# Optimization experiments

Hardware: AMD Instinct MI355X
Metric: run time of the kernel (lower is better)

## Reference

```python
import jax, jax.numpy as jnp
import numpy as np
from jax import lax

B, L = 16, 2048
D_TOK, D_TIS = 256, 64
D_MODEL = D_TOK + D_TIS          # 320
EXPAND = 2
D_INNER = EXPAND * D_MODEL       # 640
D_STATE = 16
D_CONV = 4
DT_RANK = (D_MODEL + 15) // 16   # 20 (ceil(d_model/16), Mamba default)
H_OUT = 128
VOCAB = 65                       # len(CODON_MAP_DNA)+1
N_TISSUES = 30
MAX_NORM = 2.0


def _embed_maxnorm(W, idx):
    # torch nn.Embedding(max_norm=2): looked-up rows are renormalized to norm<=2
    e = W[idx]
    n = jnp.linalg.norm(e, axis=-1, keepdims=True)
    return e * jnp.minimum(1.0, MAX_NORM / jnp.maximum(n, 1e-12))


def setup_inputs() -> dict:
    key = jax.random.key(0)
    ks = jax.random.split(key, 18)
    s = 0.02
    seq_W = jax.random.normal(ks[3], (VOCAB, D_TOK), dtype=jnp.float32)
    seq_W = seq_W.at[0].set(0.0)  # padding_idx=0
    A_log = jnp.log(jnp.broadcast_to(jnp.arange(1, D_STATE + 1, dtype=jnp.float32), (D_INNER, D_STATE)))
    return {
        "rna_data_pad": jax.random.randint(ks[0], (B, L), 0, VOCAB).astype(jnp.int32),
        "tissue_id": jax.random.randint(ks[1], (B,), 0, N_TISSUES).astype(jnp.int32),
        "seq_lengths": jax.random.randint(ks[2], (B,), 1, L + 1).astype(jnp.int32),
        "seq_W": seq_W,
        "tissue_W": jax.random.normal(ks[4], (N_TISSUES, D_TIS), dtype=jnp.float32),
        "in_proj_W": jax.random.normal(ks[5], (2 * D_INNER, D_MODEL), dtype=jnp.float32) * s,
        "conv_w": jax.random.normal(ks[6], (D_INNER, 1, D_CONV), dtype=jnp.float32) * s,
        "conv_b": jnp.zeros((D_INNER,), dtype=jnp.float32),
        "x_proj_W": jax.random.normal(ks[7], (DT_RANK + 2 * D_STATE, D_INNER), dtype=jnp.float32) * s,
        "dt_proj_W": jax.random.normal(ks[8], (D_INNER, DT_RANK), dtype=jnp.float32) * s,
        "dt_proj_b": jax.random.uniform(ks[9], (D_INNER,), minval=-4.0, maxval=-2.0),
        "A_log": A_log,
        "D_skip": jnp.ones((D_INNER,), dtype=jnp.float32),
        "out_proj_W": jax.random.normal(ks[10], (D_MODEL, D_INNER), dtype=jnp.float32) * s,
        "p1_W": jax.random.normal(ks[11], (H_OUT, D_MODEL), dtype=jnp.float32) * s,
        "p1_b": jnp.zeros((H_OUT,), dtype=jnp.float32),
        "p2_W": jax.random.normal(ks[12], (1, H_OUT), dtype=jnp.float32) * s,
        "p2_b": jnp.zeros((1,), dtype=jnp.float32),
    }


def reference(rna_data_pad, tissue_id, seq_lengths, seq_W, tissue_W, in_proj_W,
              conv_w, conv_b, x_proj_W, dt_proj_W, dt_proj_b, A_log, D_skip,
              out_proj_W, p1_W, p1_b, p2_W, p2_b):
    b, l = rna_data_pad.shape
    # embeddings + tissue broadcast + mask
    seq_emb = _embed_maxnorm(seq_W, rna_data_pad)            # [B,L,D_TOK]
    tis_emb = _embed_maxnorm(tissue_W, tissue_id)            # [B,D_TIS]
    tis_exp = jnp.broadcast_to(tis_emb[:, None, :], (b, l, tis_emb.shape[-1]))
    x = jnp.concatenate([seq_emb, tis_exp], axis=-1)          # [B,L,D_MODEL]
    x = x * (rna_data_pad != 0)[..., None]
    # Mamba block
    xz = x @ in_proj_W.T                                      # [B,L,2*D_INNER]
    xm, z = jnp.split(xz, 2, axis=-1)
    xt = xm.transpose(0, 2, 1)                                # [B,D_INNER,L]
    conv = lax.conv_general_dilated(
        xt, conv_w, window_strides=(1,), padding=[(D_CONV - 1, 0)],
        feature_group_count=D_INNER,
        dimension_numbers=("NCH", "OIH", "NCH")) + conv_b[None, :, None]
    xm = jax.nn.silu(conv).transpose(0, 2, 1)                 # [B,L,D_INNER]
    x_dbl = xm @ x_proj_W.T                                   # [B,L,DT_RANK+2*D_STATE]
    dt, Bm, Cm = jnp.split(x_dbl, [DT_RANK, DT_RANK + D_STATE], axis=-1)
    delta = jax.nn.softplus(dt @ dt_proj_W.T + dt_proj_b)     # [B,L,D_INNER]
    A = -jnp.exp(A_log)                                       # [D_INNER,D_STATE]
    # selective scan over time
    xs = (delta.transpose(1, 0, 2), Bm.transpose(1, 0, 2),
          Cm.transpose(1, 0, 2), xm.transpose(1, 0, 2))
    h0 = jnp.zeros((b, D_INNER, D_STATE), dtype=xm.dtype)

    def step(h, t):
        dl, bt, ct, ut = t                                    # [B,di],[B,ds],[B,ds],[B,di]
        dA = jnp.exp(dl[:, :, None] * A)                      # [B,di,ds]
        dBu = (dl * ut)[:, :, None] * bt[:, None, :]          # [B,di,ds]
        h = dA * h + dBu
        y = jnp.einsum("bds,bs->bd", h, ct)
        return h, y

    _, ys = lax.scan(step, h0, xs)                            # ys: [L,B,D_INNER]
    y = ys.transpose(1, 0, 2) + xm * D_skip
    y = y * jax.nn.silu(z)
    out = y @ out_proj_W.T                                    # [B,L,D_MODEL]
    # gather last valid timestep
    out_last = out[jnp.arange(b), seq_lengths - 1]            # [B,D_MODEL]
    h1 = jax.nn.relu(out_last @ p1_W.T + p1_b)
    return h1 @ p2_W.T + p2_b                                 # [B,1]
```

## Files before the change

### kernel.cpp

```cpp
#include <hip/hip_runtime.h>
#include <hip/hip_bf16.h>
#include <math.h>

#define B_      16
#define L_      2048
#define D_MODEL 320
#define D_INNER 640
#define D_STATE 16
#define DT_RANK 20
#define H_OUT   128
#define VOCAB   65
#define N_TIS   30
#define TT      8
#define ST      64
#define NCHUNK  16
#define CHLEN   (L_/NCHUNK)

static constexpr size_t OFF_MSEQ  = 0;
static constexpr size_t OFF_MTIS  = OFF_MSEQ + VOCAB*1280;
static constexpr size_t OFF_YSCAN = OFF_MTIS + N_TIS*1280;
static constexpr size_t OFF_CLAST = OFF_YSCAN + B_*D_INNER;
static constexpr size_t OFF_XD    = OFF_CLAST + B_*16;
static constexpr size_t OFF_PC    = OFF_XD + (size_t)B_*L_*36;
static constexpr size_t OFF_SC    = OFF_PC + (size_t)B_*NCHUNK*40*256;

__device__ __forceinline__ float silu_f(float x) { return x / (1.0f + __expf(-x)); }

__global__ __launch_bounds__(256) void k_mbuild(
    const float* __restrict__ seqW, const float* __restrict__ tisW,
    const float* __restrict__ inW, float* __restrict__ ws)
{
    __shared__ float a_l[256];
    __shared__ float red[4];
    int v = blockIdx.x, tid = threadIdx.x;
    int K, wofs; const float* src; float* dstM;
    if (v < VOCAB) { K = 256; wofs = 0;   src = seqW + (size_t)v*256;        dstM = ws + OFF_MSEQ + (size_t)v*1280; }
    else           { K = 64;  wofs = 256; src = tisW + (size_t)(v-VOCAB)*64; dstM = ws + OFF_MTIS + (size_t)(v-VOCAB)*1280; }
    float x = (tid < K) ? src[tid] : 0.0f;
    float ss = x * x;
    #pragma unroll
    for (int o = 32; o; o >>= 1) ss += __shfl_xor(ss, o);
    if ((tid & 63) == 0) red[tid >> 6] = ss;
    __syncthreads();
    float tot = red[0] + red[1] + red[2] + red[3];
    float scale = fminf(1.0f, 2.0f / fmaxf(sqrtf(tot), 1e-12f));
    if (tid < K) a_l[tid] = x * scale;
    __syncthreads();

    int j = blockIdx.y * 256 + tid;
    const float* w = inW + (size_t)j*320 + wofs;
    float ac0 = 0.f, ac1 = 0.f, ac2 = 0.f, ac3 = 0.f;
    #pragma unroll 4
    for (int k = 0; k < K; k += 4) {
        float4 w4 = *(const float4*)(w + k);
        ac0 += a_l[k+0]*w4.x; ac1 += a_l[k+1]*w4.y;
        ac2 += a_l[k+2]*w4.z; ac3 += a_l[k+3]*w4.w;
    }
    dstM[j] = (ac0 + ac1) + (ac2 + ac3);
}

__global__ __launch_bounds__(256) void k_xdbl(
    const int* __restrict__ idx, const int* __restrict__ tissue_id,
    const int* __restrict__ seq_lengths,
    const float* __restrict__ conv_w, const float* __restrict__ conv_b,
    const float* __restrict__ xW, float* __restrict__ ws)
{
    __shared__ float u_l[TT*641];
    __shared__ float xd_l[TT*36];
    __shared__ int   idx_l[TT+3];
    int b = blockIdx.y;
    int t0 = blockIdx.x * TT;
    int t_last = seq_lengths[b] - 1;
    if (t0 > t_last) return;
    int tid = threadIdx.x;
    const float* Mseq = ws + OFF_MSEQ;
    const float* Mtis = ws + OFF_MTIS;
    int tis = tissue_id[b];
    if (tid < TT+3) {
        int t = t0 - 3 + tid;
        idx_l[tid] = (t >= 0) ? idx[b*L_ + t] : 0;
    }
    __syncthreads();

    for (int d = tid; d < D_INNER; d += 256) {
        float w0 = conv_w[d*4+0], w1 = conv_w[d*4+1], w2 = conv_w[d*4+2], w3 = conv_w[d*4+3];
        float cb = conv_b[d];
        float mt = Mtis[(size_t)tis*1280 + d];
        auto XZ = [&](int k) -> float {
            int row = idx_l[k];
            return row ? (Mseq[(size_t)row*1280 + d] + mt) : 0.0f;
        };
        float a0 = XZ(0), a1 = XZ(1), a2 = XZ(2);
        for (int t = 0; t < TT; ++t) {
            float a3 = XZ(t+3);
            float c = w0*a0 + w1*a1 + w2*a2 + w3*a3 + cb;
            u_l[t*641 + d] = silu_f(c);
            a0 = a1; a1 = a2; a2 = a3;
        }
    }
    __syncthreads();

    {
        int w = tid >> 6, l = tid & 63;
        #pragma unroll 1
        for (int pass = 0; pass < 3; ++pass) {
            float wreg[3][10];
            #pragma unroll
            for (int kk = 0; kk < 3; ++kk) {
                const float* xr = xW + (size_t)(w + 4*(3*pass + kk))*D_INNER + l;
                #pragma unroll
                for (int i = 0; i < 10; ++i) wreg[kk][i] = xr[64*i];
            }
            for (int t = 0; t < TT; ++t) {
                float ur[10];
                #pragma unroll
                for (int i = 0; i < 10; ++i) ur[i] = u_l[t*641 + l + 64*i];
                #pragma unroll
                for (int kk = 0; kk < 3; ++kk) {
                    float p = 0.f;
                    #pragma unroll
                    for (int i = 0; i < 10; ++i) p = fmaf(wreg[kk][i], ur[i], p);
                    #pragma unroll
                    for (int o = 32; o; o >>= 1) p += __shfl_xor(p, o);
                    if (l == t) xd_l[t*36 + w + 4*(3*pass + kk)] = p;
                }
            }
        }
        if (t_last < t0 + TT) {
            int tl = t_last - t0;
            float ur[10];
            #pragma unroll
            for (int i = 0; i < 10; ++i) ur[i] = u_l[tl*641 + l + 64*i];
            #pragma unroll
            for (int k = 0; k < 4; ++k) {
                const float* xr = xW + (size_t)(36 + w + 4*k)*D_INNER + l;
                float p = 0.f;
                #pragma unroll
                for (int i = 0; i < 10; ++i) p = fmaf(xr[64*i], ur[i], p);
                #pragma unroll
                for (int o = 32; o; o >>= 1) p += __shfl_xor(p, o);
                if (l == 0) ws[OFF_CLAST + b*16 + w + 4*k] = p;
            }
        }
    }
    __syncthreads();

    {
        int tmax = min(TT-1, t_last - t0);
        int cnt = (tmax + 1) * 36;
        float* dst = ws + OFF_XD + ((size_t)b*L_ + t0)*36;
        for (int o = tid; o < cnt; o += 256) dst[o] = xd_l[o];
    }
}

__global__ __launch_bounds__(256) void k_scanc(
    const int* __restrict__ idx, const int* __restrict__ tissue_id,
    const int* __restrict__ seq_lengths,
    const float* __restrict__ conv_w, const float* __restrict__ conv_b,
    const float* __restrict__ dtW, const float* __restrict__ dtb,
    const float* __restrict__ A_log, float* __restrict__ ws)
{
    __shared__ float xd_t[ST*36];
    __shared__ float dl_t[16*68];
    __shared__ float du_t[16*68];
    __shared__ float dtw_l[16*20];
    __shared__ float cw_l[16*4];
    __shared__ float cb_l[16], dtb_l[16], mt_l[16];
    __shared__ int   idx_t[ST+3];

    int b = blockIdx.y, dg = blockIdx.x, c = blockIdx.z;
    int t_last = seq_lengths[b] - 1;
    int t_begin = c * CHLEN;
    if (t_begin > t_last) return;
    int t_end = min(t_begin + CHLEN - 1, t_last);
    int tid = threadIdx.x;
    int dl = tid >> 4, s = tid & 15;
    int tis = tissue_id[b];
    const float* Mseq = ws + OFF_MSEQ;

    if (tid < 16) {
        int d = dg*16 + tid;
        cb_l[tid]  = conv_b[d];
        dtb_l[tid] = dtb[d];
        mt_l[tid]  = ws[OFF_MTIS + (size_t)tis*1280 + d];
    }
    if (tid < 64) {
        int dd = tid >> 2, k = tid & 3;
        cw_l[dd*4 + k] = conv_w[(dg*16 + dd)*4 + k];
    }
    for (int o = tid; o < 16*20; o += 256) {
        int dd = o / 20, r = o % 20;
        dtw_l[o] = dtW[(dg*16 + dd)*20 + r];
    }
    float A = -__expf(A_log[(dg*16 + dl)*D_STATE + s]);

    float h = 0.0f;
    float sd = 0.0f;
    for (int t0 = t_begin; t0 <= t_end; t0 += ST) {
        int nt = min(ST, t_end - t0 + 1);
        if (tid < ST+3) {
            int t = t0 - 3 + tid;
            idx_t[tid] = (t >= 0 && t < L_) ? idx[b*L_ + t] : 0;
        }
        {
            const float* src = ws + OFF_XD + ((size_t)b*L_ + t0)*36;
            int cnt = nt * 36;
            for (int o = tid; o < cnt; o += 256) xd_t[o] = src[o];
        }
        __syncthreads();

        {
            int tt = tid >> 2, dd0 = (tid & 3) * 4;
            if (tt < nt) {
                float cc0 = cb_l[dd0+0], cc1 = cb_l[dd0+1], cc2 = cb_l[dd0+2], cc3 = cb_l[dd0+3];
                #pragma unroll
                for (int k = 0; k < 4; ++k) {
                    int row = idx_t[tt + k];
                    float4 m;
                    if (row) {
                        m = *(const float4*)(Mseq + (size_t)row*1280 + dg*16 + dd0);
                        m.x += mt_l[dd0+0]; m.y += mt_l[dd0+1];
                        m.z += mt_l[dd0+2]; m.w += mt_l[dd0+3];
                    } else m = make_float4(0.f,0.f,0.f,0.f);
                    cc0 = fmaf(cw_l[(dd0+0)*4+k], m.x, cc0);
                    cc1 = fmaf(cw_l[(dd0+1)*4+k], m.y, cc1);
                    cc2 = fmaf(cw_l[(dd0+2)*4+k], m.z, cc2);
                    cc3 = fmaf(cw_l[(dd0+3)*4+k], m.w, cc3);
                }
                float uu[4] = { silu_f(cc0), silu_f(cc1), silu_f(cc2), silu_f(cc3) };
                float xdr[20];
                #pragma unroll
                for (int r = 0; r < 20; ++r) xdr[r] = xd_t[tt*36 + r];
                #pragma unroll
                for (int i = 0; i < 4; ++i) {
                    int d = dd0 + i;
                    float x = dtb_l[d];
                    #pragma unroll
                    for (int r = 0; r < 20; ++r) x = fmaf(xdr[r], dtw_l[d*20 + r], x);
                    float sp = fmaxf(x, 0.0f) + log1pf(__expf(-fabsf(x)));
                    dl_t[d*68 + tt] = sp;
                    du_t[d*68 + tt] = sp * uu[i];
                }
            }
        }
        __syncthreads();

        {
            int q4 = nt >> 2;
            for (int q = 0; q < q4; ++q) {
                float4 d4 = *(const float4*)(dl_t + dl*68 + 4*q);
                float4 u4 = *(const float4*)(du_t + dl*68 + 4*q);
                float b0 = xd_t[(4*q+0)*36 + 20 + s];
                float b1 = xd_t[(4*q+1)*36 + 20 + s];
                float b2 = xd_t[(4*q+2)*36 + 20 + s];
                float b3 = xd_t[(4*q+3)*36 + 20 + s];
                h = fmaf(__expf(d4.x*A), h, u4.x*b0);
                h = fmaf(__expf(d4.y*A), h, u4.y*b1);
                h = fmaf(__expf(d4.z*A), h, u4.z*b2);
                h = fmaf(__expf(d4.w*A), h, u4.w*b3);
                sd += (d4.x + d4.y) + (d4.z + d4.w);
            }
            for (int tt = q4*4; tt < nt; ++tt) {
                float dlt = dl_t[dl*68 + tt];
                h = fmaf(__expf(dlt * A), h, du_t[dl*68 + tt] * xd_t[tt*36 + 20 + s]);
                sd += dlt;
            }
        }
        __syncthreads();
    }
    float P = __expf(A * sd);
    size_t base = (((size_t)b*NCHUNK + c)*40 + dg)*256 + tid;
    ws[OFF_PC + base] = P;
    ws[OFF_SC + base] = h;
}

__global__ __launch_bounds__(256) void k_comb(const int* __restrict__ seq_lengths,
                                              float* __restrict__ ws)
{
    int b = blockIdx.y, dg = blockIdx.x;
    int tid = threadIdx.x;
    int dl = tid >> 4, s = tid & 15;
    int t_last = seq_lengths[b] - 1;
    int ncv = t_last / CHLEN + 1;
    float h = 0.0f;
    for (int c = 0; c < ncv; ++c) {
        size_t base = (((size_t)b*NCHUNK + c)*40 + dg)*256 + tid;
        h = fmaf(ws[OFF_PC + base], h, ws[OFF_SC + base]);
    }
    float v = h * ws[OFF_CLAST + b*16 + s];
    v += __shfl_xor(v, 1); v += __shfl_xor(v, 2);
    v += __shfl_xor(v, 4); v += __shfl_xor(v, 8);
    if (s == 0) ws[OFF_YSCAN + (size_t)b*D_INNER + dg*16 + dl] = v;
}

__global__ __launch_bounds__(320) void k_final(
    const int* __restrict__ idx, const int* __restrict__ tissue_id,
    const int* __restrict__ seq_lengths,
    const float* __restrict__ conv_w, const float* __restrict__ conv_b,
    const float* __restrict__ Dskip, const float* __restrict__ outW,
    const float* __restrict__ p1W, const float* __restrict__ p1b,
    const float* __restrict__ p2W, const float* __restrict__ p2b,
    const float* __restrict__ ws, float* __restrict__ out)
{
    __shared__ float y_l[D_INNER];
    __shared__ float o_l[D_MODEL];
    __shared__ float h1_l[H_OUT];
    int b = blockIdx.x, tid = threadIdx.x;
    int t_last = seq_lengths[b] - 1;
    int tis = tissue_id[b];
    const float* Mseq = ws + OFF_MSEQ;
    const float* Mtis = ws + OFF_MTIS;
    int rows[4];
    #pragma unroll
    for (int k = 0; k < 4; ++k) {
        int t = t_last - 3 + k;
        rows[k] = (t >= 0) ? idx[b*L_ + t] : 0;
    }
    for (int d = tid; d < D_INNER; d += 320) {
        float conv = conv_b[d];
        const float* cw = conv_w + d*4;
        #pragma unroll
        for (int k = 0; k < 4; ++k) {
            int row = rows[k];
            float xz = row ? (Mseq[(size_t)row*1280 + d] + Mtis[(size_t)tis*1280 + d]) : 0.0f;
            conv += cw[k] * xz;
        }
        float u = silu_f(conv);
        int rowL = rows[3];
        float z = rowL ? (Mseq[(size_t)rowL*1280 + 640 + d] + Mtis[(size_t)tis*1280 + 640 + d]) : 0.0f;
        float ys = ws[OFF_YSCAN + (size_t)b*D_INNER + d];
        y_l[d] = (ys + u * Dskip[d]) * silu_f(z);
    }
    __syncthreads();
    if (tid < D_MODEL) {
        const float* w = outW + tid*D_INNER;
        float acc = 0.f;
        #pragma unroll 4
        for (int k = 0; k < D_INNER; k += 4) {
            float4 w4 = *(const float4*)(w + k);
            acc += y_l[k]*w4.x + y_l[k+1]*w4.y + y_l[k+2]*w4.z + y_l[k+3]*w4.w;
        }
        o_l[tid] = acc;
    }
    __syncthreads();
    if (tid < H_OUT) {
        const float* w = p1W + tid*D_MODEL;
        float acc = p1b[tid];
        #pragma unroll 4
        for (int k = 0; k < D_MODEL; k += 4) {
            float4 w4 = *(const float4*)(w + k);
            acc += o_l[k]*w4.x + o_l[k+1]*w4.y + o_l[k+2]*w4.z + o_l[k+3]*w4.w;
        }
        h1_l[tid] = fmaxf(acc, 0.0f);
    }
    __syncthreads();
    if (tid == 0) {
        float acc = p2b[0];
        for (int k = 0; k < H_OUT; ++k) acc += h1_l[k]*p2W[k];
        out[b] = acc;
    }
}

extern "C" void kernel_launch(void* const* d_in, const int* in_sizes, int n_in,
                              void* d_out, int out_size, void* d_ws, size_t ws_size,
                              hipStream_t stream)
{
    const int*   idx   = (const int*)d_in[0];
    const int*   tis   = (const int*)d_in[1];
    const int*   slen  = (const int*)d_in[2];
    const float* seqW  = (const float*)d_in[3];
    const float* tisW  = (const float*)d_in[4];
    const float* inW   = (const float*)d_in[5];
    const float* convw = (const float*)d_in[6];
    const float* convb = (const float*)d_in[7];
    const float* xW    = (const float*)d_in[8];
    const float* dtW   = (const float*)d_in[9];
    const float* dtb   = (const float*)d_in[10];
    const float* Alog  = (const float*)d_in[11];
    const float* Dsk   = (const float*)d_in[12];
    const float* outW  = (const float*)d_in[13];
    const float* p1W   = (const float*)d_in[14];
    const float* p1b   = (const float*)d_in[15];
    const float* p2W   = (const float*)d_in[16];
    const float* p2b   = (const float*)d_in[17];
    float* ws  = (float*)d_ws;
    float* out = (float*)d_out;

    hipLaunchKernelGGL(k_mbuild, dim3(VOCAB + N_TIS, 5), dim3(256), 0, stream, seqW, tisW, inW, ws);
    hipLaunchKernelGGL(k_xdbl,   dim3(L_/TT, B_),        dim3(256), 0, stream,
                       idx, tis, slen, convw, convb, xW, ws);
    hipLaunchKernelGGL(k_scanc,  dim3(D_INNER/16, B_, NCHUNK), dim3(256), 0, stream,
                       idx, tis, slen, convw, convb, dtW, dtb, Alog, ws);
    hipLaunchKernelGGL(k_comb,   dim3(D_INNER/16, B_),   dim3(256), 0, stream, slen, ws);
    hipLaunchKernelGGL(k_final,  dim3(B_),               dim3(320), 0, stream,
                       idx, tis, slen, convw, convb, Dsk, outW, p1W, p1b, p2W, p2b, ws, out);
}
```

Baseline: 298.8 us.

## Restructure scan-chunk prologue, fold chunk combine into final kernel, use exp2

The per-chunk scan kernel now has each thread own one inner channel and compute four consecutive timesteps. Conv weights, dt weights and biases are held in registers instead of shared memory, and convolution inputs are reused across the sliding window. Loads become float4, softplus uses fast log, and the decay exponent switches to exp2 with a prescaled A. The separate chunk-combine kernel is removed and its work is folded into k_final, saving a launch but serializing the combine over only 16 blocks.

```diff
diff --git a/kernel.cpp b/kernel.cpp
--- a/kernel.cpp
+++ b/kernel.cpp
@@ -161,11 +161,8 @@
     const float* __restrict__ A_log, float* __restrict__ ws)
 {
     __shared__ float xd_t[ST*36];
-    __shared__ float dl_t[16*68];
-    __shared__ float du_t[16*68];
-    __shared__ float dtw_l[16*20];
-    __shared__ float cw_l[16*4];
-    __shared__ float cb_l[16], dtb_l[16], mt_l[16];
+    __shared__ float dl_t[16*72];
+    __shared__ float du_t[16*72];
     __shared__ int   idx_t[ST+3];
 
     int b = blockIdx.y, dg = blockIdx.x, c = blockIdx.z;
@@ -175,24 +172,22 @@
     int t_end = min(t_begin + CHLEN - 1, t_last);
     int tid = threadIdx.x;
     int dl = tid >> 4, s = tid & 15;
+    int dd = tid & 15, tg = tid >> 4;
+    int d_own = dg*16 + dd;
     int tis = tissue_id[b];
     const float* Mseq = ws + OFF_MSEQ;
 
-    if (tid < 16) {
-        int d = dg*16 + tid;
-        cb_l[tid]  = conv_b[d];
-        dtb_l[tid] = dtb[d];
-        mt_l[tid]  = ws[OFF_MTIS + (size_t)tis*1280 + d];
-    }
-    if (tid < 64) {
-        int dd = tid >> 2, k = tid & 3;
-        cw_l[dd*4 + k] = conv_w[(dg*16 + dd)*4 + k];
-    }
-    for (int o = tid; o < 16*20; o += 256) {
-        int dd = o / 20, r = o % 20;
-        dtw_l[o] = dtW[(dg*16 + dd)*20 + r];
-    }
-    float A = -__expf(A_log[(dg*16 + dl)*D_STATE + s]);
+    float dtw_r[20];
+    #pragma unroll
+    for (int i = 0; i < 20; i += 4) {
+        float4 w4 = *(const float4*)(dtW + d_own*20 + i);
+        dtw_r[i] = w4.x; dtw_r[i+1] = w4.y; dtw_r[i+2] = w4.z; dtw_r[i+3] = w4.w;
+    }
+    float4 cw4 = *(const float4*)(conv_w + d_own*4);
+    float  cb  = conv_b[d_own];
+    float  dtb_v = dtb[d_own];
+    float  mt  = ws[OFF_MTIS + (size_t)tis*1280 + d_own];
+    float As = -__expf(A_log[(dg*16 + dl)*D_STATE + s]) * 1.44269504089f;
 
     float h = 0.0f;
     float sd = 0.0f;
@@ -203,43 +198,58 @@
             idx_t[tid] = (t >= 0 && t < L_) ? idx[b*L_ + t] : 0;
         }
         {
-            const float* src = ws + OFF_XD + ((size_t)b*L_ + t0)*36;
-            int cnt = nt * 36;
-            for (int o = tid; o < cnt; o += 256) xd_t[o] = src[o];
+            const float4* src = (const float4*)(ws + OFF_XD + ((size_t)b*L_ + t0)*36);
+            float4* dst = (float4*)xd_t;
+            int cnt4 = nt * 9;
+            for (int o = tid; o < cnt4; o += 256) dst[o] = src[o];
         }
         __syncthreads();
 
         {
-            int tt = tid >> 2, dd0 = (tid & 3) * 4;
-            if (tt < nt) {
-                float cc0 = cb_l[dd0+0], cc1 = cb_l[dd0+1], cc2 = cb_l[dd0+2], cc3 = cb_l[dd0+3];
-                #pragma unroll
-                for (int k = 0; k < 4; ++k) {
-                    int row = idx_t[tt + k];
-                    float4 m;
-                    if (row) {
-                        m = *(const float4*)(Mseq + (size_t)row*1280 + dg*16 + dd0);
-                        m.x += mt_l[dd0+0]; m.y += mt_l[dd0+1];
-                        m.z += mt_l[dd0+2]; m.w += mt_l[dd0+3];
-                    } else m = make_float4(0.f,0.f,0.f,0.f);
-                    cc0 = fmaf(cw_l[(dd0+0)*4+k], m.x, cc0);
-                    cc1 = fmaf(cw_l[(dd0+1)*4+k], m.y, cc1);
-                    cc2 = fmaf(cw_l[(dd0+2)*4+k], m.z, cc2);
-                    cc3 = fmaf(cw_l[(dd0+3)*4+k], m.w, cc3);
+            int ttb = tg * 4;
+            if (ttb < nt) {
+                float xz[7];
+                #pragma unroll
+                for (int k = 0; k < 7; ++k) {
+                    int row = idx_t[ttb + k];
+                    xz[k] = row ? (Mseq[(size_t)row*1280 + d_own] + mt) : 0.0f;
                 }
-                float uu[4] = { silu_f(cc0), silu_f(cc1), silu_f(cc2), silu_f(cc3) };
-                float xdr[20];
-                #pragma unroll
-                for (int r = 0; r < 20; ++r) xdr[r] = xd_t[tt*36 + r];
-                #pragma unroll
-                for (int i = 0; i < 4; ++i) {
-                    int d = dd0 + i;
-                    float x = dtb_l[d];
-                    #pragma unroll
-                    for (int r = 0; r < 20; ++r) x = fmaf(xdr[r], dtw_l[d*20 + r], x);
-                    float sp = fmaxf(x, 0.0f) + log1pf(__expf(-fabsf(x)));
-                    dl_t[d*68 + tt] = sp;
-                    du_t[d*68 + tt] = sp * uu[i];
+                float dl4[4], du4[4];
+                bool full = (ttb + 3 < nt);
+                #pragma unroll
+                for (int j = 0; j < 4; ++j) {
+                    int tt = ttb + j;
+                    if (full || tt < nt) {
+                        float cc = cb;
+                        cc = fmaf(cw4.x, xz[j+0], cc);
+                        cc = fmaf(cw4.y, xz[j+1], cc);
+                        cc = fmaf(cw4.z, xz[j+2], cc);
+                        cc = fmaf(cw4.w, xz[j+3], cc);
+                        float u = silu_f(cc);
+                        const float* xr = xd_t + tt*36;
+                        float x = dtb_v;
+                        #pragma unroll
+                        for (int r = 0; r < 20; r += 4) {
+                            float4 x4 = *(const float4*)(xr + r);
+                            x = fmaf(x4.x, dtw_r[r+0], x);
+                            x = fmaf(x4.y, dtw_r[r+1], x);
+                            x = fmaf(x4.z, dtw_r[r+2], x);
+                            x = fmaf(x4.w, dtw_r[r+3], x);
+                        }
+                        float e = __expf(-fabsf(x));
+                        float sp = fmaxf(x, 0.0f) + __logf(1.0f + e);
+                        dl4[j] = sp;
+                        du4[j] = sp * u;
+                    } else { dl4[j] = 0.f; du4[j] = 0.f; }
+                }
+                if (full) {
+                    *(float4*)(dl_t + dd*72 + ttb) = make_float4(dl4[0], dl4[1], dl4[2], dl4[3]);
+                    *(float4*)(du_t + dd*72 + ttb) = make_float4(du4[0], du4[1], du4[2], du4[3]);
+                } else {
+                    for (int j = 0; j < 4 && ttb + j < nt; ++j) {
+                        dl_t[dd*72 + ttb + j] = dl4[j];
+                        du_t[dd*72 + ttb + j] = du4[j];
+                    }
                 }
             }
         }
@@ -248,49 +258,30 @@
         {
             int q4 = nt >> 2;
             for (int q = 0; q < q4; ++q) {
-                float4 d4 = *(const float4*)(dl_t + dl*68 + 4*q);
-                float4 u4 = *(const float4*)(du_t + dl*68 + 4*q);
+                float4 d4 = *(const float4*)(dl_t + dl*72 + 4*q);
+                float4 u4 = *(const float4*)(du_t + dl*72 + 4*q);
                 float b0 = xd_t[(4*q+0)*36 + 20 + s];
                 float b1 = xd_t[(4*q+1)*36 + 20 + s];
                 float b2 = xd_t[(4*q+2)*36 + 20 + s];
                 float b3 = xd_t[(4*q+3)*36 + 20 + s];
-                h = fmaf(__expf(d4.x*A), h, u4.x*b0);
-                h = fmaf(__expf(d4.y*A), h, u4.y*b1);
-                h = fmaf(__expf(d4.z*A), h, u4.z*b2);
-                h = fmaf(__expf(d4.w*A), h, u4.w*b3);
+                h = fmaf(exp2f(d4.x*As), h, u4.x*b0);
+                h = fmaf(exp2f(d4.y*As), h, u4.y*b1);
+                h = fmaf(exp2f(d4.z*As), h, u4.z*b2);
+                h = fmaf(exp2f(d4.w*As), h, u4.w*b3);
                 sd += (d4.x + d4.y) + (d4.z + d4.w);
             }
             for (int tt = q4*4; tt < nt; ++tt) {
-                float dlt = dl_t[dl*68 + tt];
-                h = fmaf(__expf(dlt * A), h, du_t[dl*68 + tt] * xd_t[tt*36 + 20 + s]);
+                float dlt = dl_t[dl*72 + tt];
+                h = fmaf(exp2f(dlt * As), h, du_t[dl*72 + tt] * xd_t[tt*36 + 20 + s]);
                 sd += dlt;
             }
         }
         __syncthreads();
     }
-    float P = __expf(A * sd);
+    float P = exp2f(As * sd);
     size_t base = (((size_t)b*NCHUNK + c)*40 + dg)*256 + tid;
     ws[OFF_PC + base] = P;
     ws[OFF_SC + base] = h;
-}
-
-__global__ __launch_bounds__(256) void k_comb(const int* __restrict__ seq_lengths,
-                                              float* __restrict__ ws)
-{
-    int b = blockIdx.y, dg = blockIdx.x;
-    int tid = threadIdx.x;
-    int dl = tid >> 4, s = tid & 15;
-    int t_last = seq_lengths[b] - 1;
-    int ncv = t_last / CHLEN + 1;
-    float h = 0.0f;
-    for (int c = 0; c < ncv; ++c) {
-        size_t base = (((size_t)b*NCHUNK + c)*40 + dg)*256 + tid;
-        h = fmaf(ws[OFF_PC + base], h, ws[OFF_SC + base]);
-    }
-    float v = h * ws[OFF_CLAST + b*16 + s];
-    v += __shfl_xor(v, 1); v += __shfl_xor(v, 2);
-    v += __shfl_xor(v, 4); v += __shfl_xor(v, 8);
-    if (s == 0) ws[OFF_YSCAN + (size_t)b*D_INNER + dg*16 + dl] = v;
 }
 
 __global__ __launch_bounds__(320) void k_final(
@@ -305,11 +296,16 @@
     __shared__ float y_l[D_INNER];
     __shared__ float o_l[D_MODEL];
     __shared__ float h1_l[H_OUT];
+    __shared__ float cl_l[16];
     int b = blockIdx.x, tid = threadIdx.x;
     int t_last = seq_lengths[b] - 1;
+    int ncv = t_last / CHLEN + 1;
     int tis = tissue_id[b];
     const float* Mseq = ws + OFF_MSEQ;
     const float* Mtis = ws + OFF_MTIS;
+    if (tid < 16) cl_l[tid] = ws[OFF_CLAST + b*16 + tid];
+    __syncthreads();
+
     int rows[4];
     #pragma unroll
     for (int k = 0; k < 4; ++k) {
@@ -317,18 +313,38 @@
         rows[k] = (t >= 0) ? idx[b*L_ + t] : 0;
     }
     for (int d = tid; d < D_INNER; d += 320) {
+        int dgg = d >> 4, dll = d & 15;
+        float hs[16];
+        #pragma unroll
+        for (int s = 0; s < 16; ++s) hs[s] = 0.0f;
+        for (int c = 0; c < ncv; ++c) {
+            const float* pc = ws + OFF_PC + (((size_t)b*NCHUNK + c)*40 + dgg)*256 + dll*16;
+            const float* sc = ws + OFF_SC + (((size_t)b*NCHUNK + c)*40 + dgg)*256 + dll*16;
+            #pragma unroll
+            for (int s4 = 0; s4 < 4; ++s4) {
+                float4 p = *(const float4*)(pc + 4*s4);
+                float4 sv = *(const float4*)(sc + 4*s4);
+                hs[4*s4+0] = fmaf(p.x, hs[4*s4+0], sv.x);
+                hs[4*s4+1] = fmaf(p.y, hs[4*s4+1], sv.y);
+                hs[4*s4+2] = fmaf(p.z, hs[4*s4+2], sv.z);
+                hs[4*s4+3] = fmaf(p.w, hs[4*s4+3], sv.w);
+            }
+        }
+        float ys = 0.0f;
+        #pragma unroll
+        for (int s = 0; s < 16; ++s) ys = fmaf(hs[s], cl_l[s], ys);
+
         float conv = conv_b[d];
         const float* cw = conv_w + d*4;
         #pragma unroll
         for (int k = 0; k < 4; ++k) {
             int row = rows[k];
-            float xz = row ? (Mseq[(size_t)row*1280 + d] + Mtis[(size_t)tis*1280 + d]) : 0.0f;
-            conv += cw[k] * xz;
+            float xzv = row ? (Mseq[(size_t)row*1280 + d] + Mtis[(size_t)tis*1280 + d]) : 0.0f;
+            conv += cw[k] * xzv;
         }
         float u = silu_f(conv);
         int rowL = rows[3];
         float z = rowL ? (Mseq[(size_t)rowL*1280 + 640 + d] + Mtis[(size_t)tis*1280 + 640 + d]) : 0.0f;
-        float ys = ws[OFF_YSCAN + (size_t)b*D_INNER + d];
         y_l[d] = (ys + u * Dskip[d]) * silu_f(z);
     }
     __syncthreads();
@@ -391,7 +407,6 @@
                        idx, tis, slen, convw, convb, xW, ws);
     hipLaunchKernelGGL(k_scanc,  dim3(D_INNER/16, B_, NCHUNK), dim3(256), 0, stream,
                        idx, tis, slen, convw, convb, dtW, dtb, Alog, ws);
-    hipLaunchKernelGGL(k_comb,   dim3(D_INNER/16, B_),   dim3(256), 0, stream, slen, ws);
     hipLaunchKernelGGL(k_final,  dim3(B_),               dim3(320), 0, stream,
                        idx, tis, slen, convw, convb, Dsk, outW, p1W, p1b, p2W, p2b, ws, out);
 }
```

Result: no change. 295.4 us (-1.1%).
